# Optimization experiments

Measured on AMD Instinct MI355X. Metric: run time of the kernel, lower is better.

## Reference

```python
import jax, jax.numpy as jnp
import numpy as np
from jax import lax

NUM_STEPS = 10
B, D = 524288, 32


def setup_inputs() -> dict:
    key = jax.random.key(0)
    k1, k2, k3 = jax.random.split(key, 3)
    outputs = jax.random.normal(k1, (B, D), dtype=jnp.float32)
    targets = jax.random.normal(k2, (B, D), dtype=jnp.float32)
    christoffel_symbols = jax.random.normal(k3, (D, D, D), dtype=jnp.float32)
    return {"outputs": outputs, "targets": targets,
            "christoffel_symbols": christoffel_symbols}


def reference(outputs, targets, christoffel_symbols):
    gamma = christoffel_symbols
    if gamma.ndim == 2:
        gamma = gamma[None]  # mirror unsqueeze(0) in the torch code
    dt = jnp.float32(1.0 / NUM_STEPS)

    def step(carry, _):
        traj, vel = carry
        # geodesic ODE: a^i = -Gamma^i_{jk} v^j v^k  (batched)
        acc = -jnp.einsum('ijk,bj,bk->bi', gamma, vel, vel)
        vel = vel + acc * dt
        traj = traj + vel * dt
        return (traj, vel), None

    init = (outputs, jnp.zeros_like(outputs))
    (traj, _), _ = lax.scan(step, init, None, length=NUM_STEPS)
    geodesic_distance = jnp.linalg.norm(traj - targets, axis=1)  # [B]
    return jnp.mean(geodesic_distance)
```

## Files before the change

kernel.cpp:

```cpp
#include <hip/hip_runtime.h>


static constexpr int B_ROWS = 524288;
static constexpr int NUM_F4 = B_ROWS * 8;
static constexpr int BLK    = 1024;
static constexpr int NBLK   = NUM_F4 / BLK;

__global__ __launch_bounds__(1024) void geodesic_loss_kernel(
    const float4* __restrict__ o4,
    const float4* __restrict__ t4,
    float* __restrict__ out)
{
    const int idx = blockIdx.x * BLK + threadIdx.x;

    float4 o = o4[idx];
    float4 g = t4[idx];
    float dx = o.x - g.x;
    float dy = o.y - g.y;
    float dz = o.z - g.z;
    float dw = o.w - g.w;
    float s  = dx * dx + dy * dy + dz * dz + dw * dw;

    s += __shfl_xor(s, 1);
    s += __shfl_xor(s, 2);
    s += __shfl_xor(s, 4);

    float d = ((threadIdx.x & 7) == 0) ? sqrtf(s) : 0.0f;

    d += __shfl_xor(d, 8);
    d += __shfl_xor(d, 16);
    d += __shfl_xor(d, 32);

    __shared__ float sm[16];
    const int wave = threadIdx.x >> 6;
    if ((threadIdx.x & 63) == 0) sm[wave] = d;
    __syncthreads();
    if (threadIdx.x == 0) {
        float total = 0.0f;
#pragma unroll
        for (int i = 0; i < 16; ++i) total += sm[i];
        atomicAdd(out, total * (1.0f / (float)B_ROWS));
    }
}

extern "C" void kernel_launch(void* const* d_in, const int* in_sizes, int n_in,
                              void* d_out, int out_size, void* d_ws, size_t ws_size,
                              hipStream_t stream) {
    const float4* outputs = (const float4*)d_in[0];
    const float4* targets = (const float4*)d_in[1];
    float* out = (float*)d_out;

    hipMemsetAsync(out, 0, sizeof(float), stream);

    geodesic_loss_kernel<<<dim3(NBLK), dim3(BLK), 0, stream>>>(
        outputs, targets, out);
}
```

Before: 167.5 us.

## Split loss into two passes with bf16 per-row partial sums in workspace

Replaces the single fused kernel with two kernels. The first uses a grid-stride loop to compute squared-difference partials for each float4 and stores them as bf16 in the workspace. The second reads the eight partials of each row, takes the sqrt, and reduces with wave shuffles and an atomic. The intent is better load scheduling and smaller blocks, but it adds an extra launch, an intermediate write and read, and bf16 rounding error in the partial sums.

```diff
diff --git a/kernel.cpp b/kernel.cpp
--- a/kernel.cpp
+++ b/kernel.cpp
@@ -1,45 +1,66 @@
 #include <hip/hip_runtime.h>
+#include <hip/hip_bf16.h>
 
 
-static constexpr int B_ROWS = 524288;
-static constexpr int NUM_F4 = B_ROWS * 8;
-static constexpr int BLK    = 1024;
-static constexpr int NBLK   = NUM_F4 / BLK;
+static constexpr int B_ROWS  = 524288;
+static constexpr int NUM_F4  = B_ROWS * 8;
+static constexpr int P1_BLK  = 256;
+static constexpr int P1_NBLK = 2048;
+static constexpr int P1_THREADS = P1_BLK * P1_NBLK;
+static constexpr int P1_ITER = NUM_F4 / P1_THREADS;
 
-__global__ __launch_bounds__(1024) void geodesic_loss_kernel(
+typedef __attribute__((ext_vector_type(8))) unsigned short ushort8;
+
+__global__ __launch_bounds__(P1_BLK) void geodesic_pass1(
     const float4* __restrict__ o4,
     const float4* __restrict__ t4,
+    __hip_bfloat16* __restrict__ partial)
+{
+    const int gtid = blockIdx.x * P1_BLK + threadIdx.x;
+#pragma unroll
+    for (int i = 0; i < P1_ITER; ++i) {
+        const int idx = i * P1_THREADS + gtid;
+        float4 o = o4[idx];
+        float4 g = t4[idx];
+        float dx = o.x - g.x;
+        float dy = o.y - g.y;
+        float dz = o.z - g.z;
+        float dw = o.w - g.w;
+        float p  = dx * dx + dy * dy + dz * dz + dw * dw;
+        partial[idx] = __float2bfloat16(p);
+    }
+}
+
+static constexpr int P2_BLK  = 256;
+static constexpr int P2_NBLK = B_ROWS / P2_BLK;
+
+__global__ __launch_bounds__(P2_BLK) void geodesic_pass2(
+    const ushort8* __restrict__ partial8,
     float* __restrict__ out)
 {
-    const int idx = blockIdx.x * BLK + threadIdx.x;
+    const int row = blockIdx.x * P2_BLK + threadIdx.x;
+    ushort8 p = partial8[row];
 
-    float4 o = o4[idx];
-    float4 g = t4[idx];
-    float dx = o.x - g.x;
-    float dy = o.y - g.y;
-    float dz = o.z - g.z;
-    float dw = o.w - g.w;
-    float s  = dx * dx + dy * dy + dz * dz + dw * dw;
+    float ss = 0.0f;
+#pragma unroll
+    for (int j = 0; j < 8; ++j) {
+        __hip_bfloat16_raw r; r.x = p[j];
+        ss += (float)__hip_bfloat16(r);
+    }
+    float d = sqrtf(ss);
 
-    s += __shfl_xor(s, 1);
-    s += __shfl_xor(s, 2);
-    s += __shfl_xor(s, 4);
-
-    float d = ((threadIdx.x & 7) == 0) ? sqrtf(s) : 0.0f;
-
+    d += __shfl_xor(d, 1);
+    d += __shfl_xor(d, 2);
+    d += __shfl_xor(d, 4);
     d += __shfl_xor(d, 8);
     d += __shfl_xor(d, 16);
     d += __shfl_xor(d, 32);
 
-    __shared__ float sm[16];
-    const int wave = threadIdx.x >> 6;
-    if ((threadIdx.x & 63) == 0) sm[wave] = d;
+    __shared__ float sm[4];
+    if ((threadIdx.x & 63) == 0) sm[threadIdx.x >> 6] = d;
     __syncthreads();
     if (threadIdx.x == 0) {
-        float total = 0.0f;
-#pragma unroll
-        for (int i = 0; i < 16; ++i) total += sm[i];
-        atomicAdd(out, total * (1.0f / (float)B_ROWS));
+        atomicAdd(out, (sm[0] + sm[1] + sm[2] + sm[3]) * (1.0f / (float)B_ROWS));
     }
 }
 
@@ -49,9 +70,12 @@
     const float4* outputs = (const float4*)d_in[0];
     const float4* targets = (const float4*)d_in[1];
     float* out = (float*)d_out;
+    __hip_bfloat16* partial = (__hip_bfloat16*)d_ws;
 
     hipMemsetAsync(out, 0, sizeof(float), stream);
 
-    geodesic_loss_kernel<<<dim3(NBLK), dim3(BLK), 0, stream>>>(
-        outputs, targets, out);
+    geodesic_pass1<<<dim3(P1_NBLK), dim3(P1_BLK), 0, stream>>>(
+        outputs, targets, partial);
+    geodesic_pass2<<<dim3(P2_NBLK), dim3(P2_BLK), 0, stream>>>(
+        (const ushort8*)partial, out);
 }
```

Measured after the change: 177.7 us. 1.06x slower.
